# Kernel optimization log

Measured on AMD Instinct MI355X. Metric: run time of the kernel, lower is better.

## Reference

```python
import jax, jax.numpy as jnp
import numpy as np

B, C_IN, T, H, W = 32, 1024, 7, 14, 14
C_INTER = 512


def setup_inputs() -> dict:
    key = jax.random.key(0)
    ks = jax.random.split(key, 8)
    s = lambda fan_in: 1.0 / np.sqrt(fan_in)
    return {
        "x_window": jax.random.normal(ks[0], (B, C_IN, T, H, W), jnp.float32),
        "nodes": jax.random.normal(ks[1], (T, C_INTER), jnp.float32),
        "Wq": jax.random.normal(ks[2], (C_IN, C_INTER), jnp.float32) * s(C_IN),
        "bq": jnp.zeros((C_INTER,), jnp.float32),
        "Wk": jax.random.normal(ks[3], (C_INTER, C_INTER), jnp.float32) * s(C_INTER),
        "bk": jnp.zeros((C_INTER,), jnp.float32),
        "Wv": jax.random.normal(ks[4], (C_IN, C_INTER), jnp.float32) * s(C_IN),
        "bv": jnp.zeros((C_INTER,), jnp.float32),
        "Wo": jax.random.normal(ks[5], (C_INTER, C_IN), jnp.float32) * s(C_INTER),
        "bo": jnp.zeros((C_IN,), jnp.float32),
    }


def reference(x_window, nodes, Wq, bq, Wk, bk, Wv, bv, Wo, bo):
    # x_window: (B, C_in, T, H, W); dropout is identity at eval time.
    t_mid = x_window.shape[2] // 2
    x_item = x_window[:, :, t_mid]                                   # (B, C_in, H, W)
    # pointwise (Linear3d) projections over channel dim
    query = jnp.einsum("bchw,cd->bdhw", x_item, Wq) + bq[None, :, None, None]
    key = nodes @ Wk + bk                                            # (T, C_inter)
    value = jnp.einsum("bcthw,cd->bdthw", x_window, Wv) + bv[None, :, None, None, None]
    # per-pixel attention scores over the T node keys
    alpha = jnp.einsum("bdhw,td->bthw", query, key)                  # (B, T, H, W)
    alpha = jax.nn.softmax(alpha, axis=1)
    # per-pixel weighted temporal sum
    y = jnp.einsum("bthw,bdthw->bdhw", alpha, value)                 # (B, C_inter, H, W)
    out = jnp.einsum("bdhw,dc->bchw", y, Wo) + bo[None, :, None, None]
    return out[:, :, None]                                           # (B, C_in, 1, H, W)
```

## Files before the change

### kernel.cpp

```cpp
#include <hip/hip_runtime.h>
#include <hip/hip_bf16.h>
#include <stdint.h>

#define BB    32
#define CIN   1024
#define TT    7
#define HHWW  196
#define HW4   49
#define CI    512
#define TMID  3
#define MM    (BB*HHWW)
#define NCH   16
#define CSZ   64

using bf16 = __hip_bfloat16;
typedef __attribute__((ext_vector_type(8))) short short8;
typedef __attribute__((ext_vector_type(4))) short s16x4;
typedef __attribute__((ext_vector_type(4))) float f32x4;

__device__ __forceinline__ void gload_lds16(const void* g, void* l) {
    __builtin_amdgcn_global_load_lds((const __attribute__((address_space(1))) void*)g,
                                     (__attribute__((address_space(3))) void*)l, 16, 0, 0);
}

template <int EPI>
__device__ __forceinline__ void gemm_body(const bf16* __restrict__ A, const bf16* __restrict__ Bt,
                                          void* __restrict__ Cout, const float* __restrict__ bias,
                                          int M, int N, int K, int bm, int bn,
                                          bf16 (&As)[128 * 64], bf16 (&Bs)[128 * 64]) {
    int tid = threadIdx.x;
    int wid = tid >> 6, lane = tid & 63;
    int wr = wid >> 1, wc = wid & 1;
    f32x4 acc[4][4] = {};
    const bf16* Ab = A + (size_t)bm * 128 * K;
    const bf16* Bb = Bt + (size_t)bn * 128 * K;
    int row = lane & 15;
    int kb_base = (lane >> 4) * 8;

    for (int k0 = 0; k0 < K; k0 += 64) {
        #pragma unroll
        for (int it = 0; it < 4; ++it) {
            int e = (it * 256 + tid) * 8;
            int r = e >> 6, cc = e & 63;
            gload_lds16(Ab + (size_t)r * K + k0 + cc, &As[e]);
            gload_lds16(Bb + (size_t)r * K + k0 + cc, &Bs[e]);
        }
        __syncthreads();
        #pragma unroll
        for (int kk = 0; kk < 2; ++kk) {
            int kb = kk * 32 + kb_base;
            short8 a[4], b[4];
            #pragma unroll
            for (int mi = 0; mi < 4; ++mi) a[mi] = *(const short8*)&As[(wr * 64 + mi * 16 + row) * 64 + kb];
            #pragma unroll
            for (int ni = 0; ni < 4; ++ni) b[ni] = *(const short8*)&Bs[(wc * 64 + ni * 16 + row) * 64 + kb];
            #pragma unroll
            for (int mi = 0; mi < 4; ++mi)
                #pragma unroll
                for (int ni = 0; ni < 4; ++ni)
                    acc[mi][ni] = __builtin_amdgcn_mfma_f32_16x16x32_bf16(a[mi], b[ni], acc[mi][ni], 0, 0, 0);
        }
        __syncthreads();
    }

    int col_l = lane & 15, row_l = (lane >> 4) * 4;
    if constexpr (EPI == 0) {
        bf16* C = (bf16*)Cout;
        #pragma unroll
        for (int mi = 0; mi < 4; ++mi) {
            int row0 = bm * 128 + wr * 64 + mi * 16 + row_l;
            #pragma unroll
            for (int ni = 0; ni < 4; ++ni) {
                int col = bn * 128 + wc * 64 + ni * 16 + col_l;
                #pragma unroll
                for (int r = 0; r < 4; ++r)
                    C[(size_t)(row0 + r) * N + col] = __float2bfloat16(acc[mi][ni][r]);
            }
        }
    } else {
        float* Cf = (float*)Cout;
        #pragma unroll
        for (int ni = 0; ni < 4; ++ni) {
            int n = bn * 128 + wc * 64 + ni * 16 + col_l;
            float bz = bias[n];
            #pragma unroll
            for (int mi = 0; mi < 4; ++mi) {
                int m0 = bm * 128 + wr * 64 + mi * 16 + row_l;
                int b = m0 / HHWW;
                int hw0 = m0 - b * HHWW;
                f32x4 v = acc[mi][ni];
                v[0] += bz; v[1] += bz; v[2] += bz; v[3] += bz;
                *(f32x4*)&Cf[((size_t)b * CIN + n) * HHWW + hw0] = v;
            }
        }
    }
}

__global__ __launch_bounds__(256) void k_prep1(
    const float* __restrict__ nodes, const float* __restrict__ Wk, const float* __restrict__ bk,
    float* __restrict__ key,
    const float* __restrict__ Wv, const float* __restrict__ Wo,
    bf16* __restrict__ Wv_bf, bf16* __restrict__ WoT_bf,
    const float* __restrict__ bv, const float* __restrict__ bo, float* __restrict__ bvo) {
    __shared__ float sred[512];
    int bid = blockIdx.x, tid = threadIdx.x;
    if (bid < 56) {
        int t = bid >> 3, dc = bid & 7;
        int d_l = tid & 63, q = tid >> 6;
        int d = dc * 64 + d_l;
        float acc = 0.f;
        const float* nr = nodes + t * CI;
        #pragma unroll 4
        for (int c = q * 128; c < q * 128 + 128; ++c)
            acc = fmaf(nr[c], Wk[(size_t)c * CI + d], acc);
        sred[q * 64 + d_l] = acc;
        __syncthreads();
        if (q == 0)
            key[t * CI + d] = sred[d_l] + sred[64 + d_l] + sred[128 + d_l] + sred[192 + d_l] + bk[d];
    } else if (bid < 56 + 2048) {
        int i = (bid - 56) * 256 + tid;
        Wv_bf[i] = __float2bfloat16(Wv[i]);
        int d = i >> 10, cp = i & 1023;
        WoT_bf[(size_t)cp * CI + d] = __float2bfloat16(Wo[i]);
    } else {
        int cp0 = (bid - 2104) * 32;
        int cp_l = tid & 31, dq = tid >> 5;
        float acc = 0.f;
        #pragma unroll 4
        for (int d = dq * 64; d < dq * 64 + 64; ++d)
            acc = fmaf(bv[d], Wo[(size_t)d * CIN + cp0 + cp_l], acc);
        sred[dq * 32 + cp_l] = acc;
        __syncthreads();
        if (dq == 0) {
            float v = bo[cp0 + cp_l];
            #pragma unroll
            for (int g = 0; g < 8; ++g) v += sred[g * 32 + cp_l];
            bvo[cp0 + cp_l] = v;
        }
    }
}

__global__ __launch_bounds__(256) void k_prep2(
    const bf16* __restrict__ WoT_bf, const bf16* __restrict__ Wv_bf, bf16* __restrict__ WvoT,
    const float* __restrict__ Wq, const float* __restrict__ bq,
    const float* __restrict__ key, float* __restrict__ Wqk, float* __restrict__ bqk) {
    __shared__ __align__(16) bf16 As[128 * 64];
    __shared__ __align__(16) bf16 Bs[128 * 64];
    int bid = blockIdx.x;
    if (bid < 64) {
        gemm_body<0>(WoT_bf, Wv_bf, (void*)WvoT, nullptr, 1024, 1024, 512, bid >> 3, bid & 7, As, Bs);
        return;
    }
    int c = (bid - 64) * 4 + (threadIdx.x >> 6);
    int lane = threadIdx.x & 63;
    if (c > CIN) return;
    const float* src = (c < CIN) ? (Wq + (size_t)c * CI) : bq;
    float acc[TT] = {};
    #pragma unroll 2
    for (int it = 0; it < CI / 64; ++it) {
        float w = src[it * 64 + lane];
        #pragma unroll
        for (int t = 0; t < TT; ++t) acc[t] = fmaf(w, key[t * CI + it * 64 + lane], acc[t]);
    }
    #pragma unroll
    for (int t = 0; t < TT; ++t) {
        float v = acc[t];
        for (int off = 32; off; off >>= 1) v += __shfl_down(v, off);
        if (lane == 0) { if (c < CIN) Wqk[c * 8 + t] = v; else bqk[t] = v; }
    }
}

__global__ __launch_bounds__(256) void k_alpha(const float* __restrict__ x,
                                               const float* __restrict__ Wqk,
                                               float* __restrict__ part) {
    __shared__ float wq_s[CSZ * 8];
    int ch = blockIdx.x, b = blockIdx.y;
    int tid = threadIdx.x;
    for (int i = tid; i < CSZ * 8; i += 256) wq_s[i] = Wqk[ch * CSZ * 8 + i];
    __syncthreads();
    if (tid < HHWW) {
        float acc[TT] = {};
        const float* xb = x + (size_t)(b * CIN + ch * CSZ) * TT * HHWW + TMID * HHWW + tid;
        #pragma unroll 8
        for (int c = 0; c < CSZ; ++c) {
            float v = xb[(size_t)c * TT * HHWW];
            #pragma unroll
            for (int t = 0; t < TT; ++t) acc[t] = fmaf(v, wq_s[c * 8 + t], acc[t]);
        }
        #pragma unroll
        for (int t = 0; t < TT; ++t)
            part[((size_t)(b * NCH + ch) * TT + t) * HHWW + tid] = acc[t];
    }
}

__global__ __launch_bounds__(256) void k_smxw(const float* __restrict__ x,
                                              const float* __restrict__ part,
                                              const float* __restrict__ bqk,
                                              bf16* __restrict__ xw) {
    __shared__ __align__(16) float al[TT * HHWW];
    __shared__ __align__(16) bf16 txp[HHWW * 32];
    int c0 = blockIdx.x * 32;
    int b = blockIdx.y;
    int tid = threadIdx.x;
    if (tid < HHWW) {
        float s[TT];
        #pragma unroll
        for (int t = 0; t < TT; ++t) s[t] = bqk[t];
        #pragma unroll
        for (int ch = 0; ch < NCH; ++ch)
            #pragma unroll
            for (int t = 0; t < TT; ++t)
                s[t] += part[((size_t)(b * NCH + ch) * TT + t) * HHWW + tid];
        float mx = s[0];
        #pragma unroll
        for (int t = 1; t < TT; ++t) mx = fmaxf(mx, s[t]);
        float e[TT], sum = 0.f;
        #pragma unroll
        for (int t = 0; t < TT; ++t) { e[t] = __expf(s[t] - mx); sum += e[t]; }
        float inv = 1.f / sum;
        #pragma unroll
        for (int t = 0; t < TT; ++t) al[t * HHWW + tid] = e[t] * inv;
    }
    __syncthreads();
    const f32x4* xp = (const f32x4*)x;
    f32x4 acc[7] = {};
    #pragma unroll
    for (int t = 0; t < TT; ++t) {
        #pragma unroll
        for (int k = 0; k < 7; ++k) {
            int w = k * 256 + tid;
            if (k == 6 && w >= 1568) continue;
            int c_l = w / 49;
            int hw4 = w - c_l * 49;
            f32x4 a4 = *(const f32x4*)&al[t * HHWW + hw4 * 4];
            f32x4 xv = xp[((size_t)(b * CIN + c0 + c_l) * TT + t) * HW4 + hw4];
            acc[k] += a4 * xv;
        }
    }
    #pragma unroll
    for (int k = 0; k < 7; ++k) {
        int w = k * 256 + tid;
        if (k == 6 && w >= 1568) continue;
        int c_l = w / 49;
        int hw4 = w - c_l * 49;
        int v = (hw4 & 7) << 2;
        #pragma unroll
        for (int r = 0; r < 4; ++r)
            txp[(hw4 * 4 + r) * 32 + (c_l ^ v)] = __float2bfloat16(acc[k][r]);
    }
    __syncthreads();
    #pragma unroll
    for (int k = 0; k < 7; ++k) {
        int w = k * 256 + tid;
        if (k == 6 && w >= 1568) continue;
        int m = w >> 3, seg = w & 7;
        int v = ((m >> 2) & 7) << 2;
        s16x4 val = *(const s16x4*)&txp[m * 32 + ((seg * 4) ^ v)];
        *(s16x4*)&xw[(size_t)(b * HHWW + m) * CIN + c0 + seg * 4] = val;
    }
}

__global__ __launch_bounds__(256) void k_gemm1(const bf16* __restrict__ A, const bf16* __restrict__ Bt,
                                               float* __restrict__ C, const float* __restrict__ bias) {
    __shared__ __align__(16) bf16 As[128 * 64];
    __shared__ __align__(16) bf16 Bs[128 * 64];
    int id = blockIdx.x;
    int w = (id & 7) * 49 + (id >> 3);
    int bm = w >> 3, bn = w & 7;
    gemm_body<1>(A, Bt, (void*)C, bias, MM, CIN, CIN, bm, bn, As, Bs);
}

extern "C" void kernel_launch(void* const* d_in, const int* in_sizes, int n_in,
                              void* d_out, int out_size, void* d_ws, size_t ws_size,
                              hipStream_t stream) {
    const float* x     = (const float*)d_in[0];
    const float* nodes = (const float*)d_in[1];
    const float* Wq    = (const float*)d_in[2];
    const float* bq    = (const float*)d_in[3];
    const float* Wk    = (const float*)d_in[4];
    const float* bk    = (const float*)d_in[5];
    const float* Wv    = (const float*)d_in[6];
    const float* bv    = (const float*)d_in[7];
    const float* Wo    = (const float*)d_in[8];
    const float* bo    = (const float*)d_in[9];

    uint8_t* w = (uint8_t*)d_ws;
    size_t off = 0;
    auto alloc = [&](size_t bytes) -> void* {
        void* p = w + off;
        off = (off + bytes + 255) & ~(size_t)255;
        return p;
    };
    float* key    = (float*)alloc((size_t)TT * CI * 4);
    float* Wqk    = (float*)alloc((size_t)CIN * 8 * 4);
    float* bqk    = (float*)alloc(8 * 4);
    float* bvo    = (float*)alloc((size_t)CIN * 4);
    bf16*  Wv_bf  = (bf16*)alloc((size_t)CIN * CI * 2);
    bf16*  WoT_bf = (bf16*)alloc((size_t)CIN * CI * 2);
    bf16*  WvoT   = (bf16*)alloc((size_t)CIN * CIN * 2);
    float* part   = (float*)alloc((size_t)BB * NCH * TT * HHWW * 4);
    bf16*  xw     = (bf16*)alloc((size_t)MM * CIN * 2);
    (void)ws_size;

    k_prep1<<<2136, 256, 0, stream>>>(nodes, Wk, bk, key, Wv, Wo, Wv_bf, WoT_bf, bv, bo, bvo);
    k_prep2<<<321, 256, 0, stream>>>(WoT_bf, Wv_bf, WvoT, Wq, bq, key, Wqk, bqk);
    k_alpha<<<dim3(NCH, BB), 256, 0, stream>>>(x, Wqk, part);
    k_smxw<<<dim3(32, BB), 256, 0, stream>>>(x, part, bqk, xw);
    k_gemm1<<<392, 256, 0, stream>>>(xw, WvoT, (float*)d_out, bvo);
}
```

Before: 107.7 us.

## Shrink final GEMM M-tile to 64 and hoist softmax into separate kernel

The GEMM body is templated on the M tile size, and the final output GEMM now uses 64-row tiles on a 98x8 grid. This doubles the block count to improve occupancy and CU balance, and it drops the previous swizzled block ordering. The softmax over the T scores moves out of k_smxw into a new small kernel that writes alpha once per batch. Each of the 32 channel blocks then loads the precomputed alpha instead of redoing the 16-chunk reduction. The cost is one extra launch and less B-tile reuse per block in the GEMM.

```diff
diff --git a/kernel.cpp b/kernel.cpp
--- a/kernel.cpp
+++ b/kernel.cpp
@@ -23,39 +23,46 @@
                                      (__attribute__((address_space(3))) void*)l, 16, 0, 0);
 }
 
-template <int EPI>
+template <int EPI, int BM>
 __device__ __forceinline__ void gemm_body(const bf16* __restrict__ A, const bf16* __restrict__ Bt,
                                           void* __restrict__ Cout, const float* __restrict__ bias,
                                           int M, int N, int K, int bm, int bn,
-                                          bf16 (&As)[128 * 64], bf16 (&Bs)[128 * 64]) {
+                                          bf16* As, bf16* Bs) {
+    constexpr int MI = BM / 32;
+    constexpr int AIT = BM * 64 / 2048;
     int tid = threadIdx.x;
     int wid = tid >> 6, lane = tid & 63;
     int wr = wid >> 1, wc = wid & 1;
-    f32x4 acc[4][4] = {};
-    const bf16* Ab = A + (size_t)bm * 128 * K;
+    f32x4 acc[MI][4] = {};
+    const bf16* Ab = A + (size_t)bm * BM * K;
     const bf16* Bb = Bt + (size_t)bn * 128 * K;
     int row = lane & 15;
     int kb_base = (lane >> 4) * 8;
 
     for (int k0 = 0; k0 < K; k0 += 64) {
         #pragma unroll
+        for (int it = 0; it < AIT; ++it) {
+            int e = (it * 256 + tid) * 8;
+            int r = e >> 6, cc = e & 63;
+            gload_lds16(Ab + (size_t)r * K + k0 + cc, &As[e]);
+        }
+        #pragma unroll
         for (int it = 0; it < 4; ++it) {
             int e = (it * 256 + tid) * 8;
             int r = e >> 6, cc = e & 63;
-            gload_lds16(Ab + (size_t)r * K + k0 + cc, &As[e]);
             gload_lds16(Bb + (size_t)r * K + k0 + cc, &Bs[e]);
         }
         __syncthreads();
         #pragma unroll
         for (int kk = 0; kk < 2; ++kk) {
             int kb = kk * 32 + kb_base;
-            short8 a[4], b[4];
-            #pragma unroll
-            for (int mi = 0; mi < 4; ++mi) a[mi] = *(const short8*)&As[(wr * 64 + mi * 16 + row) * 64 + kb];
+            short8 a[MI], b[4];
+            #pragma unroll
+            for (int mi = 0; mi < MI; ++mi) a[mi] = *(const short8*)&As[(wr * (BM / 2) + mi * 16 + row) * 64 + kb];
             #pragma unroll
             for (int ni = 0; ni < 4; ++ni) b[ni] = *(const short8*)&Bs[(wc * 64 + ni * 16 + row) * 64 + kb];
             #pragma unroll
-            for (int mi = 0; mi < 4; ++mi)
+            for (int mi = 0; mi < MI; ++mi)
                 #pragma unroll
                 for (int ni = 0; ni < 4; ++ni)
                     acc[mi][ni] = __builtin_amdgcn_mfma_f32_16x16x32_bf16(a[mi], b[ni], acc[mi][ni], 0, 0, 0);
@@ -67,8 +74,8 @@
     if constexpr (EPI == 0) {
         bf16* C = (bf16*)Cout;
         #pragma unroll
-        for (int mi = 0; mi < 4; ++mi) {
-            int row0 = bm * 128 + wr * 64 + mi * 16 + row_l;
+        for (int mi = 0; mi < MI; ++mi) {
+            int row0 = bm * BM + wr * (BM / 2) + mi * 16 + row_l;
             #pragma unroll
             for (int ni = 0; ni < 4; ++ni) {
                 int col = bn * 128 + wc * 64 + ni * 16 + col_l;
@@ -84,8 +91,8 @@
             int n = bn * 128 + wc * 64 + ni * 16 + col_l;
             float bz = bias[n];
             #pragma unroll
-            for (int mi = 0; mi < 4; ++mi) {
-                int m0 = bm * 128 + wr * 64 + mi * 16 + row_l;
+            for (int mi = 0; mi < MI; ++mi) {
+                int m0 = bm * BM + wr * (BM / 2) + mi * 16 + row_l;
                 int b = m0 / HHWW;
                 int hw0 = m0 - b * HHWW;
                 f32x4 v = acc[mi][ni];
@@ -148,7 +155,7 @@
     __shared__ __align__(16) bf16 Bs[128 * 64];
     int bid = blockIdx.x;
     if (bid < 64) {
-        gemm_body<0>(WoT_bf, Wv_bf, (void*)WvoT, nullptr, 1024, 1024, 512, bid >> 3, bid & 7, As, Bs);
+        gemm_body<0, 128>(WoT_bf, Wv_bf, (void*)WvoT, nullptr, 1024, 1024, 512, bid >> 3, bid & 7, As, Bs);
         return;
     }
     int c = (bid - 64) * 4 + (threadIdx.x >> 6);
@@ -193,34 +200,40 @@
     }
 }
 
+__global__ __launch_bounds__(256) void k_softmaxF(const float* __restrict__ part,
+                                                  const float* __restrict__ bqk,
+                                                  float* __restrict__ alphaF) {
+    int b = blockIdx.x;
+    int tid = threadIdx.x;
+    if (tid >= HHWW) return;
+    float s[TT];
+    #pragma unroll
+    for (int t = 0; t < TT; ++t) s[t] = bqk[t];
+    #pragma unroll
+    for (int ch = 0; ch < NCH; ++ch)
+        #pragma unroll
+        for (int t = 0; t < TT; ++t)
+            s[t] += part[((size_t)(b * NCH + ch) * TT + t) * HHWW + tid];
+    float mx = s[0];
+    #pragma unroll
+    for (int t = 1; t < TT; ++t) mx = fmaxf(mx, s[t]);
+    float e[TT], sum = 0.f;
+    #pragma unroll
+    for (int t = 0; t < TT; ++t) { e[t] = __expf(s[t] - mx); sum += e[t]; }
+    float inv = 1.f / sum;
+    #pragma unroll
+    for (int t = 0; t < TT; ++t) alphaF[(size_t)b * TT * HHWW + t * HHWW + tid] = e[t] * inv;
+}
+
 __global__ __launch_bounds__(256) void k_smxw(const float* __restrict__ x,
-                                              const float* __restrict__ part,
-                                              const float* __restrict__ bqk,
+                                              const float* __restrict__ alphaF,
                                               bf16* __restrict__ xw) {
     __shared__ __align__(16) float al[TT * HHWW];
     __shared__ __align__(16) bf16 txp[HHWW * 32];
     int c0 = blockIdx.x * 32;
     int b = blockIdx.y;
     int tid = threadIdx.x;
-    if (tid < HHWW) {
-        float s[TT];
-        #pragma unroll
-        for (int t = 0; t < TT; ++t) s[t] = bqk[t];
-        #pragma unroll
-        for (int ch = 0; ch < NCH; ++ch)
-            #pragma unroll
-            for (int t = 0; t < TT; ++t)
-                s[t] += part[((size_t)(b * NCH + ch) * TT + t) * HHWW + tid];
-        float mx = s[0];
-        #pragma unroll
-        for (int t = 1; t < TT; ++t) mx = fmaxf(mx, s[t]);
-        float e[TT], sum = 0.f;
-        #pragma unroll
-        for (int t = 0; t < TT; ++t) { e[t] = __expf(s[t] - mx); sum += e[t]; }
-        float inv = 1.f / sum;
-        #pragma unroll
-        for (int t = 0; t < TT; ++t) al[t * HHWW + tid] = e[t] * inv;
-    }
+    for (int i = tid; i < TT * HHWW; i += 256) al[i] = alphaF[(size_t)b * TT * HHWW + i];
     __syncthreads();
     const f32x4* xp = (const f32x4*)x;
     f32x4 acc[7] = {};
@@ -262,12 +275,9 @@
 
 __global__ __launch_bounds__(256) void k_gemm1(const bf16* __restrict__ A, const bf16* __restrict__ Bt,
                                                float* __restrict__ C, const float* __restrict__ bias) {
-    __shared__ __align__(16) bf16 As[128 * 64];
+    __shared__ __align__(16) bf16 As[64 * 64];
     __shared__ __align__(16) bf16 Bs[128 * 64];
-    int id = blockIdx.x;
-    int w = (id & 7) * 49 + (id >> 3);
-    int bm = w >> 3, bn = w & 7;
-    gemm_body<1>(A, Bt, (void*)C, bias, MM, CIN, CIN, bm, bn, As, Bs);
+    gemm_body<1, 64>(A, Bt, (void*)C, bias, MM, CIN, CIN, blockIdx.x, blockIdx.y, As, Bs);
 }
 
 extern "C" void kernel_launch(void* const* d_in, const int* in_sizes, int n_in,
@@ -299,12 +309,14 @@
     bf16*  WoT_bf = (bf16*)alloc((size_t)CIN * CI * 2);
     bf16*  WvoT   = (bf16*)alloc((size_t)CIN * CIN * 2);
     float* part   = (float*)alloc((size_t)BB * NCH * TT * HHWW * 4);
+    float* alphaF = (float*)alloc((size_t)BB * TT * HHWW * 4);
     bf16*  xw     = (bf16*)alloc((size_t)MM * CIN * 2);
     (void)ws_size;
 
     k_prep1<<<2136, 256, 0, stream>>>(nodes, Wk, bk, key, Wv, Wo, Wv_bf, WoT_bf, bv, bo, bvo);
     k_prep2<<<321, 256, 0, stream>>>(WoT_bf, Wv_bf, WvoT, Wq, bq, key, Wqk, bqk);
     k_alpha<<<dim3(NCH, BB), 256, 0, stream>>>(x, Wqk, part);
-    k_smxw<<<dim3(32, BB), 256, 0, stream>>>(x, part, bqk, xw);
-    k_gemm1<<<392, 256, 0, stream>>>(xw, WvoT, (float*)d_out, bvo);
-}
+    k_softmaxF<<<BB, 256, 0, stream>>>(part, bqk, alphaF);
+    k_smxw<<<dim3(32, BB), 256, 0, stream>>>(x, alphaF, xw);
+    k_gemm1<<<dim3(98, 8), 256, 0, stream>>>(xw, WvoT, (float*)d_out, bvo);
+}
```

After: 108.9 us. About the same (+1.1%).

## Fuse all stages into one cooperative persistent kernel with grid syncs

Applied to the files above, without the earlier changes.

Merges the five launches into a single cooperative kernel of 512 blocks that runs each stage in turn, separated by grid-wide syncs, to remove launch gaps and tail effects between stages. Softmax is split into its own phase writing alpha to global, so the smxw stage no longer recomputes it in every block. The final GEMM loses its swizzled tile order and runs on 392 of 512 blocks. Grid syncs and the lower occupancy from launch bounds (256,2) may cost more than the launch overhead saved.

```diff
diff --git a/kernel.cpp b/kernel.cpp
--- a/kernel.cpp
+++ b/kernel.cpp
@@ -1,6 +1,9 @@
 #include <hip/hip_runtime.h>
 #include <hip/hip_bf16.h>
+#include <hip/hip_cooperative_groups.h>
 #include <stdint.h>
+
+namespace cg = cooperative_groups;
 
 #define BB    32
 #define CIN   1024
@@ -12,6 +15,7 @@
 #define MM    (BB*HHWW)
 #define NCH   16
 #define CSZ   64
+#define GRID  512
 
 using bf16 = __hip_bfloat16;
 typedef __attribute__((ext_vector_type(8))) short short8;
@@ -27,7 +31,7 @@
 __device__ __forceinline__ void gemm_body(const bf16* __restrict__ A, const bf16* __restrict__ Bt,
                                           void* __restrict__ Cout, const float* __restrict__ bias,
                                           int M, int N, int K, int bm, int bn,
-                                          bf16 (&As)[128 * 64], bf16 (&Bs)[128 * 64]) {
+                                          bf16* As, bf16* Bs) {
     int tid = threadIdx.x;
     int wid = tid >> 6, lane = tid & 63;
     int wr = wid >> 1, wc = wid & 1;
@@ -96,16 +100,15 @@
     }
 }
 
-__global__ __launch_bounds__(256) void k_prep1(
+__device__ __forceinline__ void phase_prep1_unit(
+    int u, int tid, float* sred,
     const float* __restrict__ nodes, const float* __restrict__ Wk, const float* __restrict__ bk,
     float* __restrict__ key,
     const float* __restrict__ Wv, const float* __restrict__ Wo,
     bf16* __restrict__ Wv_bf, bf16* __restrict__ WoT_bf,
     const float* __restrict__ bv, const float* __restrict__ bo, float* __restrict__ bvo) {
-    __shared__ float sred[512];
-    int bid = blockIdx.x, tid = threadIdx.x;
-    if (bid < 56) {
-        int t = bid >> 3, dc = bid & 7;
+    if (u < 56) {
+        int t = u >> 3, dc = u & 7;
         int d_l = tid & 63, q = tid >> 6;
         int d = dc * 64 + d_l;
         float acc = 0.f;
@@ -117,13 +120,13 @@
         __syncthreads();
         if (q == 0)
             key[t * CI + d] = sred[d_l] + sred[64 + d_l] + sred[128 + d_l] + sred[192 + d_l] + bk[d];
-    } else if (bid < 56 + 2048) {
-        int i = (bid - 56) * 256 + tid;
+    } else if (u < 56 + 2048) {
+        int i = (u - 56) * 256 + tid;
         Wv_bf[i] = __float2bfloat16(Wv[i]);
         int d = i >> 10, cp = i & 1023;
         WoT_bf[(size_t)cp * CI + d] = __float2bfloat16(Wo[i]);
     } else {
-        int cp0 = (bid - 2104) * 32;
+        int cp0 = (u - 2104) * 32;
         int cp_l = tid & 31, dq = tid >> 5;
         float acc = 0.f;
         #pragma unroll 4
@@ -140,19 +143,12 @@
     }
 }
 
-__global__ __launch_bounds__(256) void k_prep2(
-    const bf16* __restrict__ WoT_bf, const bf16* __restrict__ Wv_bf, bf16* __restrict__ WvoT,
+__device__ __forceinline__ void phase_wqk_unit(
+    int cbase, int tid,
     const float* __restrict__ Wq, const float* __restrict__ bq,
     const float* __restrict__ key, float* __restrict__ Wqk, float* __restrict__ bqk) {
-    __shared__ __align__(16) bf16 As[128 * 64];
-    __shared__ __align__(16) bf16 Bs[128 * 64];
-    int bid = blockIdx.x;
-    if (bid < 64) {
-        gemm_body<0>(WoT_bf, Wv_bf, (void*)WvoT, nullptr, 1024, 1024, 512, bid >> 3, bid & 7, As, Bs);
-        return;
-    }
-    int c = (bid - 64) * 4 + (threadIdx.x >> 6);
-    int lane = threadIdx.x & 63;
+    int c = cbase + (tid >> 6);
+    int lane = tid & 63;
     if (c > CIN) return;
     const float* src = (c < CIN) ? (Wq + (size_t)c * CI) : bq;
     float acc[TT] = {};
@@ -170,12 +166,9 @@
     }
 }
 
-__global__ __launch_bounds__(256) void k_alpha(const float* __restrict__ x,
-                                               const float* __restrict__ Wqk,
-                                               float* __restrict__ part) {
-    __shared__ float wq_s[CSZ * 8];
-    int ch = blockIdx.x, b = blockIdx.y;
-    int tid = threadIdx.x;
+__device__ __forceinline__ void phase_alpha_unit(
+    int ch, int b, int tid, float* wq_s,
+    const float* __restrict__ x, const float* __restrict__ Wqk, float* __restrict__ part) {
     for (int i = tid; i < CSZ * 8; i += 256) wq_s[i] = Wqk[ch * CSZ * 8 + i];
     __syncthreads();
     if (tid < HHWW) {
@@ -193,34 +186,33 @@
     }
 }
 
-__global__ __launch_bounds__(256) void k_smxw(const float* __restrict__ x,
-                                              const float* __restrict__ part,
-                                              const float* __restrict__ bqk,
-                                              bf16* __restrict__ xw) {
-    __shared__ __align__(16) float al[TT * HHWW];
-    __shared__ __align__(16) bf16 txp[HHWW * 32];
-    int c0 = blockIdx.x * 32;
-    int b = blockIdx.y;
-    int tid = threadIdx.x;
-    if (tid < HHWW) {
-        float s[TT];
-        #pragma unroll
-        for (int t = 0; t < TT; ++t) s[t] = bqk[t];
-        #pragma unroll
-        for (int ch = 0; ch < NCH; ++ch)
-            #pragma unroll
-            for (int t = 0; t < TT; ++t)
-                s[t] += part[((size_t)(b * NCH + ch) * TT + t) * HHWW + tid];
-        float mx = s[0];
-        #pragma unroll
-        for (int t = 1; t < TT; ++t) mx = fmaxf(mx, s[t]);
-        float e[TT], sum = 0.f;
-        #pragma unroll
-        for (int t = 0; t < TT; ++t) { e[t] = __expf(s[t] - mx); sum += e[t]; }
-        float inv = 1.f / sum;
-        #pragma unroll
-        for (int t = 0; t < TT; ++t) al[t * HHWW + tid] = e[t] * inv;
-    }
+__device__ __forceinline__ void phase_softmax_unit(
+    int b, int tid,
+    const float* __restrict__ part, const float* __restrict__ bqk, float* __restrict__ alphaF) {
+    if (tid >= HHWW) return;
+    float s[TT];
+    #pragma unroll
+    for (int t = 0; t < TT; ++t) s[t] = bqk[t];
+    #pragma unroll
+    for (int ch = 0; ch < NCH; ++ch)
+        #pragma unroll
+        for (int t = 0; t < TT; ++t)
+            s[t] += part[((size_t)(b * NCH + ch) * TT + t) * HHWW + tid];
+    float mx = s[0];
+    #pragma unroll
+    for (int t = 1; t < TT; ++t) mx = fmaxf(mx, s[t]);
+    float e[TT], sum = 0.f;
+    #pragma unroll
+    for (int t = 0; t < TT; ++t) { e[t] = __expf(s[t] - mx); sum += e[t]; }
+    float inv = 1.f / sum;
+    #pragma unroll
+    for (int t = 0; t < TT; ++t) alphaF[(size_t)b * TT * HHWW + t * HHWW + tid] = e[t] * inv;
+}
+
+__device__ __forceinline__ void phase_smxw_unit(
+    int c0, int b, int tid, float* al, bf16* txp,
+    const float* __restrict__ x, const float* __restrict__ alphaF, bf16* __restrict__ xw) {
+    for (int i = tid; i < TT * HHWW; i += 256) al[i] = alphaF[(size_t)b * TT * HHWW + i];
     __syncthreads();
     const f32x4* xp = (const f32x4*)x;
     f32x4 acc[7] = {};
@@ -260,14 +252,98 @@
     }
 }
 
+__global__ __launch_bounds__(256, 2) void mega(
+    const float* __restrict__ x, const float* __restrict__ nodes,
+    const float* __restrict__ Wq, const float* __restrict__ bq,
+    const float* __restrict__ Wk, const float* __restrict__ bk,
+    const float* __restrict__ Wv, const float* __restrict__ bv,
+    const float* __restrict__ Wo, const float* __restrict__ bo,
+    float* __restrict__ key, float* __restrict__ Wqk, float* __restrict__ bqk,
+    float* __restrict__ bvo, bf16* __restrict__ Wv_bf, bf16* __restrict__ WoT_bf,
+    bf16* __restrict__ WvoT, float* __restrict__ part, float* __restrict__ alphaF,
+    bf16* __restrict__ xw, float* __restrict__ out) {
+
+    cg::grid_group grid = cg::this_grid();
+    __shared__ __align__(16) char smem[32768];
+    bf16* As = (bf16*)smem;
+    bf16* Bs = (bf16*)(smem + 16384);
+    int gid = blockIdx.x, tid = threadIdx.x;
+
+    for (int u = gid; u < 2136; u += GRID) {
+        __syncthreads();
+        phase_prep1_unit(u, tid, (float*)smem, nodes, Wk, bk, key, Wv, Wo, Wv_bf, WoT_bf, bv, bo, bvo);
+    }
+    grid.sync();
+
+    if (gid < 64) {
+        gemm_body<0>(WoT_bf, Wv_bf, (void*)WvoT, nullptr, 1024, 1024, 512, gid >> 3, gid & 7, As, Bs);
+    } else if (gid < 321) {
+        phase_wqk_unit((gid - 64) * 4, tid, Wq, bq, key, Wqk, bqk);
+    }
+    grid.sync();
+
+    phase_alpha_unit(gid & 15, gid >> 4, tid, (float*)smem, x, Wqk, part);
+    grid.sync();
+
+    if (gid < BB) phase_softmax_unit(gid, tid, part, bqk, alphaF);
+    grid.sync();
+
+    for (int u = gid; u < 1024; u += GRID) {
+        __syncthreads();
+        phase_smxw_unit((u & 31) * 32, u >> 5, tid, (float*)smem, (bf16*)(smem + 5504), x, alphaF, xw);
+    }
+    grid.sync();
+
+    if (gid < 392)
+        gemm_body<1>(xw, WvoT, (void*)out, bvo, MM, CIN, CIN, gid >> 3, gid & 7, As, Bs);
+}
+
+__global__ __launch_bounds__(256) void k_prep1(
+    const float* __restrict__ nodes, const float* __restrict__ Wk, const float* __restrict__ bk,
+    float* __restrict__ key, const float* __restrict__ Wv, const float* __restrict__ Wo,
+    bf16* __restrict__ Wv_bf, bf16* __restrict__ WoT_bf,
+    const float* __restrict__ bv, const float* __restrict__ bo, float* __restrict__ bvo) {
+    __shared__ float sred[256];
+    phase_prep1_unit(blockIdx.x, threadIdx.x, sred, nodes, Wk, bk, key, Wv, Wo, Wv_bf, WoT_bf, bv, bo, bvo);
+}
+
+__global__ __launch_bounds__(256) void k_prep2(
+    const bf16* __restrict__ WoT_bf, const bf16* __restrict__ Wv_bf, bf16* __restrict__ WvoT,
+    const float* __restrict__ Wq, const float* __restrict__ bq,
+    const float* __restrict__ key, float* __restrict__ Wqk, float* __restrict__ bqk) {
+    __shared__ __align__(16) bf16 As[128 * 64];
+    __shared__ __align__(16) bf16 Bs[128 * 64];
+    int bid = blockIdx.x;
+    if (bid < 64) gemm_body<0>(WoT_bf, Wv_bf, (void*)WvoT, nullptr, 1024, 1024, 512, bid >> 3, bid & 7, As, Bs);
+    else phase_wqk_unit((bid - 64) * 4, threadIdx.x, Wq, bq, key, Wqk, bqk);
+}
+
+__global__ __launch_bounds__(256) void k_alpha(const float* __restrict__ x,
+                                               const float* __restrict__ Wqk,
+                                               float* __restrict__ part) {
+    __shared__ float wq_s[CSZ * 8];
+    phase_alpha_unit(blockIdx.x, blockIdx.y, threadIdx.x, wq_s, x, Wqk, part);
+}
+
+__global__ __launch_bounds__(256) void k_softmaxF(const float* __restrict__ part,
+                                                  const float* __restrict__ bqk,
+                                                  float* __restrict__ alphaF) {
+    phase_softmax_unit(blockIdx.x, threadIdx.x, part, bqk, alphaF);
+}
+
+__global__ __launch_bounds__(256) void k_smxw(const float* __restrict__ x,
+                                              const float* __restrict__ alphaF,
+                                              bf16* __restrict__ xw) {
+    __shared__ __align__(16) float al[TT * HHWW];
+    __shared__ __align__(16) bf16 txp[HHWW * 32];
+    phase_smxw_unit(blockIdx.x * 32, blockIdx.y, threadIdx.x, al, txp, x, alphaF, xw);
+}
+
 __global__ __launch_bounds__(256) void k_gemm1(const bf16* __restrict__ A, const bf16* __restrict__ Bt,
                                                float* __restrict__ C, const float* __restrict__ bias) {
     __shared__ __align__(16) bf16 As[128 * 64];
     __shared__ __align__(16) bf16 Bs[128 * 64];
-    int id = blockIdx.x;
-    int w = (id & 7) * 49 + (id >> 3);
-    int bm = w >> 3, bn = w & 7;
-    gemm_body<1>(A, Bt, (void*)C, bias, MM, CIN, CIN, bm, bn, As, Bs);
+    gemm_body<1>(A, Bt, (void*)C, bias, MM, CIN, CIN, blockIdx.x, blockIdx.y, As, Bs);
 }
 
 extern "C" void kernel_launch(void* const* d_in, const int* in_sizes, int n_in,
@@ -299,12 +375,41 @@
     bf16*  WoT_bf = (bf16*)alloc((size_t)CIN * CI * 2);
     bf16*  WvoT   = (bf16*)alloc((size_t)CIN * CIN * 2);
     float* part   = (float*)alloc((size_t)BB * NCH * TT * HHWW * 4);
+    float* alphaF = (float*)alloc((size_t)BB * TT * HHWW * 4);
     bf16*  xw     = (bf16*)alloc((size_t)MM * CIN * 2);
+    float* outp   = (float*)d_out;
     (void)ws_size;
+
+    bool use_coop = false;
+    int dev = 0;
+    if (hipGetDevice(&dev) == hipSuccess) {
+        int coop = 0, ncu = 0, nb = 0;
+        hipDeviceGetAttribute(&coop, hipDeviceAttributeCooperativeLaunch, dev);
+        hipDeviceGetAttribute(&ncu, hipDeviceAttributeMultiprocessorCount, dev);
+        if (coop == 1 &&
+            hipOccupancyMaxActiveBlocksPerMultiprocessor(&nb, (const void*)mega, 256, 0) == hipSuccess &&
+            nb * ncu >= GRID) {
+            use_coop = true;
+        }
+    }
+
+    if (use_coop) {
+        void* kargs[] = {
+            (void*)&x, (void*)&nodes, (void*)&Wq, (void*)&bq, (void*)&Wk, (void*)&bk,
+            (void*)&Wv, (void*)&bv, (void*)&Wo, (void*)&bo,
+            (void*)&key, (void*)&Wqk, (void*)&bqk, (void*)&bvo,
+            (void*)&Wv_bf, (void*)&WoT_bf, (void*)&WvoT, (void*)&part, (void*)&alphaF,
+            (void*)&xw, (void*)&outp
+        };
+        if (hipLaunchCooperativeKernel((const void*)mega, dim3(GRID), dim3(256), kargs, 0, stream)
+            == hipSuccess)
+            return;
+    }
 
     k_prep1<<<2136, 256, 0, stream>>>(nodes, Wk, bk, key, Wv, Wo, Wv_bf, WoT_bf, bv, bo, bvo);
     k_prep2<<<321, 256, 0, stream>>>(WoT_bf, Wv_bf, WvoT, Wq, bq, key, Wqk, bqk);
     k_alpha<<<dim3(NCH, BB), 256, 0, stream>>>(x, Wqk, part);
-    k_smxw<<<dim3(32, BB), 256, 0, stream>>>(x, part, bqk, xw);
-    k_gemm1<<<392, 256, 0, stream>>>(xw, WvoT, (float*)d_out, bvo);
-}
+    k_softmaxF<<<BB, 256, 0, stream>>>(part, bqk, alphaF);
+    k_smxw<<<dim3(32, BB), 256, 0, stream>>>(x, alphaF, xw);
+    k_gemm1<<<dim3(49, 8), 256, 0, stream>>>(xw, WvoT, (float*)d_out, bvo);
+}
```

Measured after the change: 101.3 us. 1.06x faster.

## Double-buffer GEMM LDS tiles and split softmax into separate kernel

Applied to the files above, without the earlier changes.

The shared GEMM body now double-buffers the A/B tiles in LDS and issues loads for the next K-slice before computing the current one. This overlaps global-to-LDS traffic with MFMA work and drops one barrier per iteration. The softmax over the partial scores moves out of k_smxw into a new k_softmaxF kernel, so each of the 32 channel blocks per batch no longer recomputes it. The gemm1 grid also becomes a plain 2D launch without the earlier swizzle. The trade-offs are doubled LDS per block (lower occupancy), an extra kernel launch and round trip through memory, and possibly worse L2 locality from dropping the swizzle.

```diff
diff --git a/kernel.cpp b/kernel.cpp
--- a/kernel.cpp
+++ b/kernel.cpp
@@ -27,7 +27,7 @@
 __device__ __forceinline__ void gemm_body(const bf16* __restrict__ A, const bf16* __restrict__ Bt,
                                           void* __restrict__ Cout, const float* __restrict__ bias,
                                           int M, int N, int K, int bm, int bn,
-                                          bf16 (&As)[128 * 64], bf16 (&Bs)[128 * 64]) {
+                                          bf16* As, bf16* Bs) {
     int tid = threadIdx.x;
     int wid = tid >> 6, lane = tid & 63;
     int wr = wid >> 1, wc = wid & 1;
@@ -37,30 +37,38 @@
     int row = lane & 15;
     int kb_base = (lane >> 4) * 8;
 
-    for (int k0 = 0; k0 < K; k0 += 64) {
+    auto stage = [&](int buf, int k0) {
         #pragma unroll
         for (int it = 0; it < 4; ++it) {
             int e = (it * 256 + tid) * 8;
             int r = e >> 6, cc = e & 63;
-            gload_lds16(Ab + (size_t)r * K + k0 + cc, &As[e]);
-            gload_lds16(Bb + (size_t)r * K + k0 + cc, &Bs[e]);
-        }
+            gload_lds16(Ab + (size_t)r * K + k0 + cc, &As[buf * 8192 + e]);
+            gload_lds16(Bb + (size_t)r * K + k0 + cc, &Bs[buf * 8192 + e]);
+        }
+    };
+
+    stage(0, 0);
+    int cur = 0;
+    for (int k0 = 0; k0 < K; k0 += 64) {
         __syncthreads();
+        if (k0 + 64 < K) stage(cur ^ 1, k0 + 64);
+        bf16* Ac = &As[cur * 8192];
+        bf16* Bc = &Bs[cur * 8192];
         #pragma unroll
         for (int kk = 0; kk < 2; ++kk) {
             int kb = kk * 32 + kb_base;
             short8 a[4], b[4];
             #pragma unroll
-            for (int mi = 0; mi < 4; ++mi) a[mi] = *(const short8*)&As[(wr * 64 + mi * 16 + row) * 64 + kb];
-            #pragma unroll
-            for (int ni = 0; ni < 4; ++ni) b[ni] = *(const short8*)&Bs[(wc * 64 + ni * 16 + row) * 64 + kb];
+            for (int mi = 0; mi < 4; ++mi) a[mi] = *(const short8*)&Ac[(wr * 64 + mi * 16 + row) * 64 + kb];
+            #pragma unroll
+            for (int ni = 0; ni < 4; ++ni) b[ni] = *(const short8*)&Bc[(wc * 64 + ni * 16 + row) * 64 + kb];
             #pragma unroll
             for (int mi = 0; mi < 4; ++mi)
                 #pragma unroll
                 for (int ni = 0; ni < 4; ++ni)
                     acc[mi][ni] = __builtin_amdgcn_mfma_f32_16x16x32_bf16(a[mi], b[ni], acc[mi][ni], 0, 0, 0);
         }
-        __syncthreads();
+        cur ^= 1;
     }
 
     int col_l = lane & 15, row_l = (lane >> 4) * 4;
@@ -102,10 +110,10 @@
     const float* __restrict__ Wv, const float* __restrict__ Wo,
     bf16* __restrict__ Wv_bf, bf16* __restrict__ WoT_bf,
     const float* __restrict__ bv, const float* __restrict__ bo, float* __restrict__ bvo) {
-    __shared__ float sred[512];
-    int bid = blockIdx.x, tid = threadIdx.x;
-    if (bid < 56) {
-        int t = bid >> 3, dc = bid & 7;
+    __shared__ float sred[256];
+    int u = blockIdx.x, tid = threadIdx.x;
+    if (u < 56) {
+        int t = u >> 3, dc = u & 7;
         int d_l = tid & 63, q = tid >> 6;
         int d = dc * 64 + d_l;
         float acc = 0.f;
@@ -117,13 +125,13 @@
         __syncthreads();
         if (q == 0)
             key[t * CI + d] = sred[d_l] + sred[64 + d_l] + sred[128 + d_l] + sred[192 + d_l] + bk[d];
-    } else if (bid < 56 + 2048) {
-        int i = (bid - 56) * 256 + tid;
+    } else if (u < 56 + 2048) {
+        int i = (u - 56) * 256 + tid;
         Wv_bf[i] = __float2bfloat16(Wv[i]);
         int d = i >> 10, cp = i & 1023;
         WoT_bf[(size_t)cp * CI + d] = __float2bfloat16(Wo[i]);
     } else {
-        int cp0 = (bid - 2104) * 32;
+        int cp0 = (u - 2104) * 32;
         int cp_l = tid & 31, dq = tid >> 5;
         float acc = 0.f;
         #pragma unroll 4
@@ -144,8 +152,8 @@
     const bf16* __restrict__ WoT_bf, const bf16* __restrict__ Wv_bf, bf16* __restrict__ WvoT,
     const float* __restrict__ Wq, const float* __restrict__ bq,
     const float* __restrict__ key, float* __restrict__ Wqk, float* __restrict__ bqk) {
-    __shared__ __align__(16) bf16 As[128 * 64];
-    __shared__ __align__(16) bf16 Bs[128 * 64];
+    __shared__ __align__(16) bf16 As[2 * 128 * 64];
+    __shared__ __align__(16) bf16 Bs[2 * 128 * 64];
     int bid = blockIdx.x;
     if (bid < 64) {
         gemm_body<0>(WoT_bf, Wv_bf, (void*)WvoT, nullptr, 1024, 1024, 512, bid >> 3, bid & 7, As, Bs);
@@ -193,34 +201,40 @@
     }
 }
 
+__global__ __launch_bounds__(256) void k_softmaxF(const float* __restrict__ part,
+                                                  const float* __restrict__ bqk,
+                                                  float* __restrict__ alphaF) {
+    int b = blockIdx.x;
+    int tid = threadIdx.x;
+    if (tid >= HHWW) return;
+    float s[TT];
+    #pragma unroll
+    for (int t = 0; t < TT; ++t) s[t] = bqk[t];
+    #pragma unroll
+    for (int ch = 0; ch < NCH; ++ch)
+        #pragma unroll
+        for (int t = 0; t < TT; ++t)
+            s[t] += part[((size_t)(b * NCH + ch) * TT + t) * HHWW + tid];
+    float mx = s[0];
+    #pragma unroll
+    for (int t = 1; t < TT; ++t) mx = fmaxf(mx, s[t]);
+    float e[TT], sum = 0.f;
+    #pragma unroll
+    for (int t = 0; t < TT; ++t) { e[t] = __expf(s[t] - mx); sum += e[t]; }
+    float inv = 1.f / sum;
+    #pragma unroll
+    for (int t = 0; t < TT; ++t) alphaF[(size_t)b * TT * HHWW + t * HHWW + tid] = e[t] * inv;
+}
+
 __global__ __launch_bounds__(256) void k_smxw(const float* __restrict__ x,
-                                              const float* __restrict__ part,
-                                              const float* __restrict__ bqk,
+                                              const float* __restrict__ alphaF,
                                               bf16* __restrict__ xw) {
     __shared__ __align__(16) float al[TT * HHWW];
     __shared__ __align__(16) bf16 txp[HHWW * 32];
     int c0 = blockIdx.x * 32;
     int b = blockIdx.y;
     int tid = threadIdx.x;
-    if (tid < HHWW) {
-        float s[TT];
-        #pragma unroll
-        for (int t = 0; t < TT; ++t) s[t] = bqk[t];
-        #pragma unroll
-        for (int ch = 0; ch < NCH; ++ch)
-            #pragma unroll
-            for (int t = 0; t < TT; ++t)
-                s[t] += part[((size_t)(b * NCH + ch) * TT + t) * HHWW + tid];
-        float mx = s[0];
-        #pragma unroll
-        for (int t = 1; t < TT; ++t) mx = fmaxf(mx, s[t]);
-        float e[TT], sum = 0.f;
-        #pragma unroll
-        for (int t = 0; t < TT; ++t) { e[t] = __expf(s[t] - mx); sum += e[t]; }
-        float inv = 1.f / sum;
-        #pragma unroll
-        for (int t = 0; t < TT; ++t) al[t * HHWW + tid] = e[t] * inv;
-    }
+    for (int i = tid; i < TT * HHWW; i += 256) al[i] = alphaF[(size_t)b * TT * HHWW + i];
     __syncthreads();
     const f32x4* xp = (const f32x4*)x;
     f32x4 acc[7] = {};
@@ -262,12 +276,9 @@
 
 __global__ __launch_bounds__(256) void k_gemm1(const bf16* __restrict__ A, const bf16* __restrict__ Bt,
                                                float* __restrict__ C, const float* __restrict__ bias) {
-    __shared__ __align__(16) bf16 As[128 * 64];
-    __shared__ __align__(16) bf16 Bs[128 * 64];
-    int id = blockIdx.x;
-    int w = (id & 7) * 49 + (id >> 3);
-    int bm = w >> 3, bn = w & 7;
-    gemm_body<1>(A, Bt, (void*)C, bias, MM, CIN, CIN, bm, bn, As, Bs);
+    __shared__ __align__(16) bf16 As[2 * 128 * 64];
+    __shared__ __align__(16) bf16 Bs[2 * 128 * 64];
+    gemm_body<1>(A, Bt, (void*)C, bias, MM, CIN, CIN, blockIdx.x, blockIdx.y, As, Bs);
 }
 
 extern "C" void kernel_launch(void* const* d_in, const int* in_sizes, int n_in,
@@ -299,12 +310,14 @@
     bf16*  WoT_bf = (bf16*)alloc((size_t)CIN * CI * 2);
     bf16*  WvoT   = (bf16*)alloc((size_t)CIN * CIN * 2);
     float* part   = (float*)alloc((size_t)BB * NCH * TT * HHWW * 4);
+    float* alphaF = (float*)alloc((size_t)BB * TT * HHWW * 4);
     bf16*  xw     = (bf16*)alloc((size_t)MM * CIN * 2);
     (void)ws_size;
 
     k_prep1<<<2136, 256, 0, stream>>>(nodes, Wk, bk, key, Wv, Wo, Wv_bf, WoT_bf, bv, bo, bvo);
     k_prep2<<<321, 256, 0, stream>>>(WoT_bf, Wv_bf, WvoT, Wq, bq, key, Wqk, bqk);
     k_alpha<<<dim3(NCH, BB), 256, 0, stream>>>(x, Wqk, part);
-    k_smxw<<<dim3(32, BB), 256, 0, stream>>>(x, part, bqk, xw);
-    k_gemm1<<<392, 256, 0, stream>>>(xw, WvoT, (float*)d_out, bvo);
-}
+    k_softmaxF<<<BB, 256, 0, stream>>>(part, bqk, alphaF);
+    k_smxw<<<dim3(32, BB), 256, 0, stream>>>(x, alphaF, xw);
+    k_gemm1<<<dim3(49, 8), 256, 0, stream>>>(xw, WvoT, (float*)d_out, bvo);
+}
```

Result: faster. 98.53 us (-8.5%).
